# Kernel optimization log

Hardware: AMD Instinct MI355X
Metric: run time of the kernel (lower is better)

## Reference

```python
import jax, jax.numpy as jnp
import numpy as np

B, L, H, NH = 2, 256, 512, 8
DH = H // NH
MAXLEN = 256           # module's max_seq_len; pe index offset
PE_ROWS = 2 * MAXLEN + 1


def _lin(x, W, b):
    # torch nn.Linear convention: y = x @ W.T + b
    return x @ W.T + b


def setup_inputs() -> dict:
    rng = jax.random.key(0)
    ks = jax.random.split(rng, 24)
    s = 0.02
    inp = {
        "key": jax.random.normal(ks[0], (B, L, H), jnp.float32),
        "query": jax.random.normal(ks[1], (B, L, H), jnp.float32),
        "value": jax.random.normal(ks[2], (B, L, H), jnp.float32),
        # learned params
        "pe": jax.random.normal(ks[3], (PE_ROWS, H), jnp.float32) * s,
        "Wf": jax.random.normal(ks[4], (H, 4 * H), jnp.float32) * s,
        "bf": jnp.zeros((H,), jnp.float32),
        "Wk": jax.random.normal(ks[5], (H, H), jnp.float32) * s,
        "bk": jnp.zeros((H,), jnp.float32),
        "Wq": jax.random.normal(ks[6], (H, H), jnp.float32) * s,
        "bq": jnp.zeros((H,), jnp.float32),
        "Wv": jax.random.normal(ks[7], (H, H), jnp.float32) * s,
        "bv": jnp.zeros((H,), jnp.float32),
        "Wr": jax.random.normal(ks[8], (H, H), jnp.float32) * s,
        "br": jnp.zeros((H,), jnp.float32),
        "Wo": jax.random.normal(ks[9], (H, H), jnp.float32) * s,  # ff_final
        "bo": jnp.zeros((H,), jnp.float32),
        "u": jax.random.normal(ks[10], (NH, DH), jnp.float32) * s,
        "v": jax.random.normal(ks[11], (NH, DH), jnp.float32) * s,
        # int inputs
        "seq_len": jax.random.randint(ks[12], (B,), 100, 200).astype(jnp.int64),
        "lex_num": jax.random.randint(ks[13], (B,), 0, 50).astype(jnp.int64),
    }
    pos_s = jax.random.randint(ks[14], (B, L), 0, 250)
    pos_e = pos_s + jax.random.randint(ks[15], (B, L), 0, 5)
    inp["pos_s"] = pos_s.astype(jnp.int64)
    inp["pos_e"] = pos_e.astype(jnp.int64)
    return inp


def reference(key, query, value, pe, Wf, bf, Wk, bk, Wq, bq, Wv, bv, Wr, br,
              Wo, bo, u, v, seq_len, lex_num, pos_s, pos_e):
    b, l, _ = key.shape
    # four relative position matrices [B, L, L]
    pos_ss = pos_s[:, :, None] - pos_s[:, None, :]
    pos_se = pos_s[:, :, None] - pos_e[:, None, :]
    pos_es = pos_e[:, :, None] - pos_s[:, None, :]
    pos_ee = pos_e[:, :, None] - pos_e[:, None, :]
    # gather pe embeddings, each [B, L, L, H]
    pe_ss = pe[pos_ss + MAXLEN]
    pe_se = pe[pos_se + MAXLEN]
    pe_es = pe[pos_es + MAXLEN]
    pe_ee = pe[pos_ee + MAXLEN]
    pe_4 = jnp.concatenate([pe_ss, pe_se, pe_es, pe_ee], axis=-1)  # [B,L,L,4H]
    rel = jax.nn.relu(_lin(pe_4, Wf, bf))                          # 'ff' fusion -> [B,L,L,H]

    q = _lin(query, Wq, bq).reshape(b, l, NH, DH).transpose(0, 2, 1, 3)  # [B,nh,L,dh]
    k = _lin(key, Wk, bk).reshape(b, l, NH, DH).transpose(0, 2, 1, 3)
    val = _lin(value, Wv, bv).reshape(b, l, NH, DH).transpose(0, 2, 1, 3)
    rel = _lin(rel, Wr, br).reshape(b, l, l, NH, DH)               # [B,L,L,nh,dh]

    A = jnp.einsum('bhid,bhjd->bhij', q, k)
    B_ = jnp.einsum('bhid,bijhd->bhij', q, rel)
    C = jnp.einsum('hd,bhjd->bhj', u, k)[:, :, None, :]
    D = jnp.einsum('hd,bijhd->bhij', v, rel)

    score = (A + B_ + C + D) / np.float32(np.sqrt(DH))
    total_len = seq_len + lex_num                                   # [B]
    mask = (jnp.arange(l)[None, :] < total_len[:, None])[:, None, None, :]
    score = jnp.where(mask, score, jnp.float32(-1e15))
    attn = jax.nn.softmax(score, axis=-1)
    out = jnp.einsum('bhij,bhjd->bhid', attn, val)                  # [B,nh,L,dh]
    out = out.transpose(0, 2, 1, 3).reshape(b, l, H)
    return _lin(out, Wo, bo)
```

## Files before the change

### kernel.cpp

```cpp
#include <hip/hip_runtime.h>
#include <hip/hip_bf16.h>

typedef unsigned short USHORT;
typedef long long LL;
typedef short s8v __attribute__((ext_vector_type(8)));
typedef float f32x4 __attribute__((ext_vector_type(4)));


__device__ __forceinline__ float bf2f(USHORT u) {
  union { unsigned int i; float f; } v; v.i = ((unsigned int)u) << 16; return v.f;
}
__device__ __forceinline__ USHORT f2bf(float f) {
  unsigned int x = __float_as_uint(f);
  return (USHORT)((x + 0x7fffu + ((x >> 16) & 1u)) >> 16);
}

struct PrepArgs {
  const void* fsrc[18]; USHORT* fdst[18]; int fn[18];
  const void* wr_src; USHORT* wrT;
  const void* isrc[4]; int* idst[4];
};

__global__ __launch_bounds__(256) void prep_k(PrepArgs a, const void* qraw, int* flags) {
  __shared__ int s_w;
  const int t = threadIdx.x;
  if (t == 0) s_w = 0;
  __syncthreads();
  const USHORT* qb = (const USHORT*)qraw;
  int wild = 0;
  for (int c = t; c < 512; c += 256) {
    float x = bf2f(qb[c]);
    if (!(fabsf(x) <= 1024.0f)) wild = 1;
  }
  if (wild) atomicAdd(&s_w, 1);
  __syncthreads();
  const int f = (s_w == 0) ? 1 : 0;

  const int y = blockIdx.y;
  if (y < 18) {
    const int n = a.fn[y];
    const USHORT* sb = (const USHORT*)a.fsrc[y];
    const float* sf = (const float*)a.fsrc[y];
    USHORT* d = a.fdst[y];
    for (int idx = blockIdx.x * 256 + t; idx < n; idx += gridDim.x * 256)
      d[idx] = f ? sb[idx] : f2bf(sf[idx]);
  } else if (y == 18) {
    const USHORT* sb = (const USHORT*)a.wr_src;
    const float* sf = (const float*)a.wr_src;
    for (int idx = blockIdx.x * 256 + t; idx < 262144; idx += gridDim.x * 256) {
      const int e = idx >> 9, dd = idx & 511;
      const int s = dd * 512 + e;
      a.wrT[idx] = f ? sb[s] : f2bf(sf[s]);
    }
  } else if (blockIdx.x == 0) {
    if (t == 0) flags[0] = f;
    const int fi = (((const int*)a.isrc[0])[1] == 0) ? 1 : 0;
    if (t < 2) {
      a.idst[0][t] = fi ? (int)((const LL*)a.isrc[0])[t] : ((const int*)a.isrc[0])[t];
      a.idst[1][t] = fi ? (int)((const LL*)a.isrc[1])[t] : ((const int*)a.isrc[1])[t];
    }
    for (int c = t; c < 512; c += 256) {
      a.idst[2][c] = fi ? (int)((const LL*)a.isrc[2])[c] : ((const int*)a.isrc[2])[c];
      a.idst[3][c] = fi ? (int)((const LL*)a.isrc[3])[c] : ((const int*)a.isrc[3])[c];
    }
  }
}

struct GDesc {
  const USHORT* A; const USHORT* W; const USHORT* bias;
  void* out;
  int M, N, K, lda, ldw, koff, ldo, mode, trans, pad;
};
struct GArgs { GDesc d[32]; };

__global__ __launch_bounds__(256) void gemm2_k(GArgs ga, const int* __restrict__ flags) {
  const GDesc de = ga.d[blockIdx.z];
  const int row0 = blockIdx.y * 64, col0 = blockIdx.x * 64;
  if (row0 >= de.M || col0 >= de.N) return;
  const int wave = threadIdx.x >> 6, lane = threadIdx.x & 63;
  const int mrow = row0 + wave * 16 + (lane & 15);
  const int kq = (lane >> 4) * 8;
  const bool mok = (mrow < de.M);
  const USHORT* ar = de.A + (long)(mok ? mrow : row0) * de.lda + kq;
  const int nc = col0 + (lane & 15);
  const USHORT* w0p = de.W + (long)(nc +  0) * de.ldw + de.koff + kq;
  const USHORT* w1p = de.W + (long)(nc + 16) * de.ldw + de.koff + kq;
  const USHORT* w2p = de.W + (long)(nc + 32) * de.ldw + de.koff + kq;
  const USHORT* w3p = de.W + (long)(nc + 48) * de.ldw + de.koff + kq;

  f32x4 acc[4] = {};
#pragma unroll 4
  for (int k0 = 0; k0 < de.K; k0 += 32) {
    s8v a = *(const s8v*)(ar + k0);
    s8v wv0 = *(const s8v*)(w0p + k0);
    s8v wv1 = *(const s8v*)(w1p + k0);
    s8v wv2 = *(const s8v*)(w2p + k0);
    s8v wv3 = *(const s8v*)(w3p + k0);
    acc[0] = __builtin_amdgcn_mfma_f32_16x16x32_bf16(a, wv0, acc[0], 0, 0, 0);
    acc[1] = __builtin_amdgcn_mfma_f32_16x16x32_bf16(a, wv1, acc[1], 0, 0, 0);
    acc[2] = __builtin_amdgcn_mfma_f32_16x16x32_bf16(a, wv2, acc[2], 0, 0, 0);
    acc[3] = __builtin_amdgcn_mfma_f32_16x16x32_bf16(a, wv3, acc[3], 0, 0, 0);
  }

  const int obf = (de.mode == 2) ? flags[0] : (de.mode == 1);
  const int mbase = row0 + wave * 16 + (lane >> 4) * 4;
#pragma unroll
  for (int nt = 0; nt < 4; nt++) {
    const int n = col0 + nt * 16 + (lane & 15);
    const float bias = de.bias ? bf2f(de.bias[n]) : 0.f;
#pragma unroll
    for (int r = 0; r < 4; r++) {
      const int m = mbase + r;
      if (m >= de.M) continue;
      const float vo = acc[nt][r] + bias;
      const long off = de.trans ? ((long)n * de.ldo + m) : ((long)m * de.ldo + n);
      if (obf) ((USHORT*)de.out)[off] = f2bf(vo);
      else     ((float*)de.out)[off] = vo;
    }
  }
}

__global__ __launch_bounds__(256) void mid_k(
    const USHORT* __restrict__ Ptab, const USHORT* __restrict__ q_n,
    const USHORT* __restrict__ k_n, const USHORT* __restrict__ WrT,
    const USHORT* __restrict__ u_bf, const USHORT* __restrict__ v_bf,
    const USHORT* __restrict__ br_bf,
    USHORT* __restrict__ T,
    float* __restrict__ cbv, float* __restrict__ uk, USHORT* __restrict__ vwr)
{
  const int bid = blockIdx.x, t = threadIdx.x, gsz = gridDim.x;
  const long TS = 513l * 512;
  for (int r = bid; r < 12825; r += gsz) {
    const int S0 = r / 25, rem = r % 25, di = rem / 5, dj = rem % 5;
    const USHORT* p1 = Ptab + (long)S0 * 512;
    const USHORT* p2 = Ptab + TS + (long)max(S0 - dj, 0) * 512;
    const USHORT* p3 = Ptab + 2 * TS + (long)min(S0 + di, 512) * 512;
    const USHORT* p4 = Ptab + 3 * TS + (long)min(max(S0 + di - dj, 0), 512) * 512;
    USHORT* to = T + (long)r * 512;
    const int e = t * 2;
    ushort2 x1 = *(const ushort2*)(p1 + e);
    ushort2 x2 = *(const ushort2*)(p2 + e);
    ushort2 x3 = *(const ushort2*)(p3 + e);
    ushort2 x4 = *(const ushort2*)(p4 + e);
    ushort2 o;
    o.x = f2bf(fmaxf(bf2f(x1.x) + bf2f(x2.x) + bf2f(x3.x) + bf2f(x4.x), 0.f));
    o.y = f2bf(fmaxf(bf2f(x1.y) + bf2f(x2.y) + bf2f(x3.y) + bf2f(x4.y), 0.f));
    *(ushort2*)(to + e) = o;
  }
  for (int idx = bid * 256 + t; idx < 262144; idx += gsz * 256) {
    const int hd = idx & 511;
    float s = (bf2f(q_n[idx]) + bf2f(v_bf[hd])) * bf2f(br_bf[hd]);
    float s2 = bf2f(k_n[idx]) * bf2f(u_bf[hd]);
#pragma unroll
    for (int off = 32; off > 0; off >>= 1) { s += __shfl_xor(s, off); s2 += __shfl_xor(s2, off); }
    if ((t & 63) == 0) { cbv[idx >> 6] = s; uk[idx >> 6] = s2; }
  }
  for (int o = bid * 256 + t; o < 4096; o += gsz * 256) {
    const int h = o >> 9, e = o & 511;
    float s = 0.f;
    const USHORT* wrow = WrT + (long)e * 512 + h * 64;
    const USHORT* vrow = v_bf + h * 64;
#pragma unroll
    for (int d = 0; d < 64; d += 4) {
      ushort4 wv = *(const ushort4*)(wrow + d);
      ushort4 vv = *(const ushort4*)(vrow + d);
      s += bf2f(vv.x) * bf2f(wv.x) + bf2f(vv.y) * bf2f(wv.y) +
           bf2f(vv.z) * bf2f(wv.z) + bf2f(vv.w) * bf2f(wv.w);
    }
    vwr[o] = f2bf(s);
  }
}

__global__ __launch_bounds__(1024) void score6_k(
    const USHORT* __restrict__ T,
    const float* __restrict__ cbv, const float* __restrict__ uk,
    const USHORT* __restrict__ wbuf, const float* __restrict__ S_AC,
    const USHORT* __restrict__ v_t,
    const int* __restrict__ seq_len, const int* __restrict__ lex_num,
    const int* __restrict__ pos_s, const int* __restrict__ pos_e,
    USHORT* __restrict__ out_pre)
{
  __shared__ float att[8 * 256];
  __shared__ float red[4][4];
  const int i = blockIdx.x, b = blockIdx.y, t = threadIdx.x;
  const int wave = t >> 6, lane = t & 63;
  int tl = seq_len[b] + lex_num[b];
  tl = min(max(tl, 1), 256);

  const int j0 = wave * 16;
  if (j0 < tl) {
    const int n = lane & 15, q = lane >> 4;
    const int psi = pos_s[b * 256 + i], pei = pos_e[b * 256 + i];
    const int j = j0 + n;
    const int psj = pos_s[b * 256 + j], pej = pos_e[b * 256 + j];
    const int S0 = min(max(psi - psj + 256, 0), 512);
    const int di = min(max(pei - psi, 0), 4);
    const int dj = min(max(pej - psj, 0), 4);
    const USHORT* tp = T + ((long)(S0 * 25 + di * 5 + dj)) * 512 + q * 8;
    const USHORT* wr = wbuf + ((long)((b * 8 + (n & 7)) * 256 + i)) * 512 + q * 8;
    f32x4 acc = {0.f, 0.f, 0.f, 0.f};
#pragma unroll
    for (int kk = 0; kk < 16; kk++) {
      s8v av = *(const s8v*)(tp + kk * 32);
      s8v wv = *(const s8v*)(wr + kk * 32);
      acc = __builtin_amdgcn_mfma_f32_16x16x32_bf16(av, wv, acc, 0, 0, 0);
    }
    if (n < 8) {
      const long base = (long)(b * 8 + n) * 256 + i;
      const float cb = cbv[(long)(b * 256 + i) * 8 + n];
      const float4 sac = *(const float4*)(S_AC + base * 256 + j0 + q * 4);
      const float* sacp = (const float*)&sac;
#pragma unroll
      for (int r = 0; r < 4; r++) {
        const int jr = j0 + q * 4 + r;
        att[n * 256 + jr] = (acc[r] + sacp[r] + cb + uk[(long)(b * 256 + jr) * 8 + n]) * 0.125f;
      }
    }
  }
  __syncthreads();

  const int hg = t >> 8, tj = t & 255, wig = wave & 3;
#pragma unroll
  for (int hh = 0; hh < 2; hh++) {
    const int h = hg + 4 * hh;
    const float val = (tj < tl) ? att[h * 256 + tj] : -3.0e38f;
    float m = val;
#pragma unroll
    for (int off = 32; off > 0; off >>= 1) m = fmaxf(m, __shfl_xor(m, off));
    if (lane == 0) red[hg][wig] = m;
    __syncthreads();
    m = fmaxf(fmaxf(red[hg][0], red[hg][1]), fmaxf(red[hg][2], red[hg][3]));
    const float pv = (tj < tl) ? __expf(val - m) : 0.f;
    float s = pv;
#pragma unroll
    for (int off = 32; off > 0; off >>= 1) s += __shfl_xor(s, off);
    __syncthreads();
    if (lane == 0) red[hg][wig] = s;
    __syncthreads();
    s = red[hg][0] + red[hg][1] + red[hg][2] + red[hg][3];
    if (!(s > 1e-30f)) s = 1.f;
    att[h * 256 + tj] = pv / s;
    __syncthreads();
  }

  if (t < 512) {
    const int h = t >> 6, d = t & 63;
    const USHORT* vrow = v_t + (long)(h * 64 + d) * 512 + b * 256;
    const float* arow = &att[h * 256];
    float acc = 0.f;
    const int tl4 = (tl + 3) & ~3;
    for (int jj = 0; jj < tl4; jj += 4) {
      ushort4 vv = *(const ushort4*)(vrow + jj);
      acc += arow[jj + 0] * bf2f(vv.x) + arow[jj + 1] * bf2f(vv.y) +
             arow[jj + 2] * bf2f(vv.z) + arow[jj + 3] * bf2f(vv.w);
    }
    out_pre[(long)(b * 256 + i) * 512 + h * 64 + d] = f2bf(acc);
  }
}

extern "C" void kernel_launch(void* const* d_in, const int* in_sizes, int n_in,
                              void* d_out, int out_size, void* d_ws, size_t ws_size,
                              hipStream_t stream) {
  (void)in_sizes; (void)n_in; (void)out_size; (void)ws_size;

  char* w = (char*)d_ws;
  auto take = [&](size_t n) { char* r = w; w += (n + 255) & ~(size_t)255; return r; };

  int* flags   = (int*)take(16);
  int* c_seq   = (int*)take(16);
  int* c_lex   = (int*)take(16);
  int* c_pos_s = (int*)take(2048);
  int* c_pos_e = (int*)take(2048);
  const int ns[18] = {262144,262144,262144,262656,1048576,512,262144,512,262144,512,
                      262144,512,262144,512,262144,512,512,512};
  USHORT* canon[18];
  for (int i = 0; i < 18; i++) canon[i] = (USHORT*)take((size_t)ns[i] * 2);
  USHORT* WrT     = (USHORT*)take((size_t)262144 * 2);
  USHORT* q_n     = (USHORT*)take((size_t)262144 * 2);
  USHORT* k_n     = (USHORT*)take((size_t)262144 * 2);
  USHORT* v_t     = (USHORT*)take((size_t)262144 * 2);
  USHORT* wbuf    = (USHORT*)take((size_t)2097152 * 2);
  USHORT* Ptab    = (USHORT*)take((size_t)1050624 * 2);
  USHORT* T       = (USHORT*)take((size_t)12825 * 512 * 2);
  USHORT* vwr     = (USHORT*)take((size_t)4096 * 2);
  USHORT* out_pre = (USHORT*)take((size_t)262144 * 2);
  float* S   = (float*)take((size_t)1048576 * 4);
  float* cbv = (float*)take((size_t)4096 * 4);
  float* uk  = (float*)take((size_t)4096 * 4);

  PrepArgs pa;
  for (int i = 0; i < 18; i++) { pa.fsrc[i] = d_in[i]; pa.fdst[i] = canon[i]; pa.fn[i] = ns[i]; }
  pa.wr_src = d_in[12]; pa.wrT = WrT;
  for (int i = 0; i < 4; i++) pa.isrc[i] = d_in[18 + i];
  pa.idst[0] = c_seq; pa.idst[1] = c_lex; pa.idst[2] = c_pos_s; pa.idst[3] = c_pos_e;
  prep_k<<<dim3(64, 20), 256, 0, stream>>>(pa, d_in[1], flags);

  GArgs gA = {};
  for (int z = 0; z < 4; z++)
    gA.d[z] = {canon[3], canon[4], (z == 0) ? canon[5] : nullptr, Ptab + (long)z * 513 * 512,
               513, 512, 512, 512, 2048, z * 512, 512, 1, 0, 0};
  gA.d[4] = {canon[1], canon[8],  canon[9],  q_n, 512, 512, 512, 512, 512, 0, 512, 1, 0, 0};
  gA.d[5] = {canon[0], canon[6],  canon[7],  k_n, 512, 512, 512, 512, 512, 0, 512, 1, 0, 0};
  gA.d[6] = {canon[2], canon[10], canon[11], v_t, 512, 512, 512, 512, 512, 0, 512, 1, 1, 0};
  gemm2_k<<<dim3(8, 9, 7), 256, 0, stream>>>(gA, flags);

  mid_k<<<512, 256, 0, stream>>>(Ptab, q_n, k_n, WrT, canon[16], canon[17], canon[13],
                                 T, cbv, uk, vwr);

  GArgs gB = {};
  for (int z = 0; z < 16; z++) {
    const int b = z >> 3, h = z & 7;
    gB.d[z] = {q_n + b * 131072 + h * 64, WrT, vwr + h * 512, wbuf + (long)z * 131072,
               256, 512, 64, 512, 512, h * 64, 512, 1, 0, 0};
  }
  for (int z = 0; z < 16; z++) {
    const int b = z >> 3, h = z & 7;
    gB.d[16 + z] = {q_n + b * 131072 + h * 64, k_n + b * 131072 + h * 64, nullptr,
                    S + (long)z * 65536, 256, 256, 64, 512, 512, 0, 256, 0, 0, 0};
  }
  gemm2_k<<<dim3(8, 4, 32), 256, 0, stream>>>(gB, flags);

  score6_k<<<dim3(256, 2), 1024, 0, stream>>>(
      T, cbv, uk, wbuf, S, v_t, c_seq, c_lex, c_pos_s, c_pos_e, out_pre);

  GArgs gC = {};
  gC.d[0] = {out_pre, canon[14], canon[15], d_out, 512, 512, 512, 512, 512, 0, 512, 2, 0, 0};
  gemm2_k<<<dim3(8, 8, 1), 256, 0, stream>>>(gC, flags);
}
```

Baseline: 216.8 us.

## Merge mid-stage elementwise work into the batched GEMM launch and move vWr into prep

Removes the separate mid_k launch. Its T-table build and the cbv/uk reductions now run in extra blocks of a combined g2mid_k kernel, alongside the per-head GEMM tiles, using a hand-mapped block index. The v·Wr product (vwr) is computed in a new prep_k block row that reads raw Wr directly, and the unused canonical Wr copy is skipped. This cuts one kernel launch and its serialization, and lets the independent elementwise work overlap with the GEMMs. The cost is a strided, uncoalesced read of Wr in prep and fixed block partitioning inside the combined kernel.

```diff
diff --git a/kernel.cpp b/kernel.cpp
--- a/kernel.cpp
+++ b/kernel.cpp
@@ -17,7 +17,7 @@
 
 struct PrepArgs {
   const void* fsrc[18]; USHORT* fdst[18]; int fn[18];
-  const void* wr_src; USHORT* wrT;
+  const void* wr_src; USHORT* wrT; USHORT* vwr;
   const void* isrc[4]; int* idst[4];
 };
 
@@ -38,6 +38,7 @@
 
   const int y = blockIdx.y;
   if (y < 18) {
+    if (y == 12) return;
     const int n = a.fn[y];
     const USHORT* sb = (const USHORT*)a.fsrc[y];
     const float* sf = (const float*)a.fsrc[y];
@@ -52,6 +53,29 @@
       const int s = dd * 512 + e;
       a.wrT[idx] = f ? sb[s] : f2bf(sf[s]);
     }
+  } else if (y == 19) {
+    const int o = blockIdx.x * 256 + t;
+    if (o < 4096) {
+      const int h = o >> 9, e = o & 511;
+      const USHORT* wb = (const USHORT*)a.wr_src;
+      const float* wf = (const float*)a.wr_src;
+      const USHORT* vb = (const USHORT*)a.fsrc[17];
+      const float* vf = (const float*)a.fsrc[17];
+      float s = 0.f;
+#pragma unroll 4
+      for (int d = 0; d < 64; d += 4) {
+        float acc4 = 0.f;
+#pragma unroll
+        for (int dd = 0; dd < 4; dd++) {
+          const int hd = h * 64 + d + dd;
+          const float vv = bf2f(f ? vb[hd] : f2bf(vf[hd]));
+          const float wv = bf2f(f ? wb[(long)hd * 512 + e] : f2bf(wf[(long)hd * 512 + e]));
+          acc4 += vv * wv;
+        }
+        s += acc4;
+      }
+      a.vwr[o] = f2bf(s);
+    }
   } else if (blockIdx.x == 0) {
     if (t == 0) flags[0] = f;
     const int fi = (((const int*)a.isrc[0])[1] == 0) ? 1 : 0;
@@ -73,11 +97,10 @@
 };
 struct GArgs { GDesc d[32]; };
 
-__global__ __launch_bounds__(256) void gemm2_k(GArgs ga, const int* __restrict__ flags) {
-  const GDesc de = ga.d[blockIdx.z];
-  const int row0 = blockIdx.y * 64, col0 = blockIdx.x * 64;
+__device__ __forceinline__ void gemm_tile(const GDesc& de, int row0, int col0, int t,
+                                          const int* __restrict__ flags) {
   if (row0 >= de.M || col0 >= de.N) return;
-  const int wave = threadIdx.x >> 6, lane = threadIdx.x & 63;
+  const int wave = t >> 6, lane = t & 63;
   const int mrow = row0 + wave * 16 + (lane & 15);
   const int kq = (lane >> 4) * 8;
   const bool mok = (mrow < de.M);
@@ -120,54 +143,52 @@
   }
 }
 
-__global__ __launch_bounds__(256) void mid_k(
-    const USHORT* __restrict__ Ptab, const USHORT* __restrict__ q_n,
-    const USHORT* __restrict__ k_n, const USHORT* __restrict__ WrT,
+__global__ __launch_bounds__(256) void gemm2_k(GArgs ga, const int* __restrict__ flags) {
+  gemm_tile(ga.d[blockIdx.z], blockIdx.y * 64, blockIdx.x * 64, threadIdx.x, flags);
+}
+
+__global__ __launch_bounds__(256) void g2mid_k(
+    GArgs ga, const USHORT* __restrict__ Ptab,
+    const USHORT* __restrict__ q_n, const USHORT* __restrict__ k_n,
     const USHORT* __restrict__ u_bf, const USHORT* __restrict__ v_bf,
     const USHORT* __restrict__ br_bf,
-    USHORT* __restrict__ T,
-    float* __restrict__ cbv, float* __restrict__ uk, USHORT* __restrict__ vwr)
+    USHORT* __restrict__ T, float* __restrict__ cbv, float* __restrict__ uk,
+    const int* __restrict__ flags)
 {
-  const int bid = blockIdx.x, t = threadIdx.x, gsz = gridDim.x;
-  const long TS = 513l * 512;
-  for (int r = bid; r < 12825; r += gsz) {
-    const int S0 = r / 25, rem = r % 25, di = rem / 5, dj = rem % 5;
-    const USHORT* p1 = Ptab + (long)S0 * 512;
-    const USHORT* p2 = Ptab + TS + (long)max(S0 - dj, 0) * 512;
-    const USHORT* p3 = Ptab + 2 * TS + (long)min(S0 + di, 512) * 512;
-    const USHORT* p4 = Ptab + 3 * TS + (long)min(max(S0 + di - dj, 0), 512) * 512;
-    USHORT* to = T + (long)r * 512;
-    const int e = t * 2;
-    ushort2 x1 = *(const ushort2*)(p1 + e);
-    ushort2 x2 = *(const ushort2*)(p2 + e);
-    ushort2 x3 = *(const ushort2*)(p3 + e);
-    ushort2 x4 = *(const ushort2*)(p4 + e);
-    ushort2 o;
-    o.x = f2bf(fmaxf(bf2f(x1.x) + bf2f(x2.x) + bf2f(x3.x) + bf2f(x4.x), 0.f));
-    o.y = f2bf(fmaxf(bf2f(x1.y) + bf2f(x2.y) + bf2f(x3.y) + bf2f(x4.y), 0.f));
-    *(ushort2*)(to + e) = o;
-  }
-  for (int idx = bid * 256 + t; idx < 262144; idx += gsz * 256) {
-    const int hd = idx & 511;
-    float s = (bf2f(q_n[idx]) + bf2f(v_bf[hd])) * bf2f(br_bf[hd]);
-    float s2 = bf2f(k_n[idx]) * bf2f(u_bf[hd]);
-#pragma unroll
-    for (int off = 32; off > 0; off >>= 1) { s += __shfl_xor(s, off); s2 += __shfl_xor(s2, off); }
-    if ((t & 63) == 0) { cbv[idx >> 6] = s; uk[idx >> 6] = s2; }
-  }
-  for (int o = bid * 256 + t; o < 4096; o += gsz * 256) {
-    const int h = o >> 9, e = o & 511;
-    float s = 0.f;
-    const USHORT* wrow = WrT + (long)e * 512 + h * 64;
-    const USHORT* vrow = v_bf + h * 64;
-#pragma unroll
-    for (int d = 0; d < 64; d += 4) {
-      ushort4 wv = *(const ushort4*)(wrow + d);
-      ushort4 vv = *(const ushort4*)(vrow + d);
-      s += bf2f(vv.x) * bf2f(wv.x) + bf2f(vv.y) * bf2f(wv.y) +
-           bf2f(vv.z) * bf2f(wv.z) + bf2f(vv.w) * bf2f(wv.w);
-    }
-    vwr[o] = f2bf(s);
+  const int bid = blockIdx.x, t = threadIdx.x;
+  if (bid < 768) {
+    int z, uy, ux;
+    if (bid < 512) { z = bid >> 5; const int tile = bid & 31; ux = tile >> 2; uy = tile & 3; }
+    else { const int b2 = bid - 512; z = 16 + (b2 >> 4); const int tile = b2 & 15; ux = tile >> 2; uy = tile & 3; }
+    gemm_tile(ga.d[z], uy * 64, ux * 64, t, flags);
+  } else if (bid < 896) {
+    const long TS = 513l * 512;
+    for (int r = bid - 768; r < 12825; r += 128) {
+      const int S0 = r / 25, rem = r % 25, di = rem / 5, dj = rem % 5;
+      const USHORT* p1 = Ptab + (long)S0 * 512;
+      const USHORT* p2 = Ptab + TS + (long)max(S0 - dj, 0) * 512;
+      const USHORT* p3 = Ptab + 2 * TS + (long)min(S0 + di, 512) * 512;
+      const USHORT* p4 = Ptab + 3 * TS + (long)min(max(S0 + di - dj, 0), 512) * 512;
+      USHORT* to = T + (long)r * 512;
+      const int e = t * 2;
+      ushort2 x1 = *(const ushort2*)(p1 + e);
+      ushort2 x2 = *(const ushort2*)(p2 + e);
+      ushort2 x3 = *(const ushort2*)(p3 + e);
+      ushort2 x4 = *(const ushort2*)(p4 + e);
+      ushort2 o;
+      o.x = f2bf(fmaxf(bf2f(x1.x) + bf2f(x2.x) + bf2f(x3.x) + bf2f(x4.x), 0.f));
+      o.y = f2bf(fmaxf(bf2f(x1.y) + bf2f(x2.y) + bf2f(x3.y) + bf2f(x4.y), 0.f));
+      *(ushort2*)(to + e) = o;
+    }
+  } else {
+    for (int idx = (bid - 896) * 256 + t; idx < 262144; idx += 64 * 256) {
+      const int hd = idx & 511;
+      float s = (bf2f(q_n[idx]) + bf2f(v_bf[hd])) * bf2f(br_bf[hd]);
+      float s2 = bf2f(k_n[idx]) * bf2f(u_bf[hd]);
+#pragma unroll
+      for (int off = 32; off > 0; off >>= 1) { s += __shfl_xor(s, off); s2 += __shfl_xor(s2, off); }
+      if ((t & 63) == 0) { cbv[idx >> 6] = s; uk[idx >> 6] = s2; }
+    }
   }
 }
 
@@ -274,7 +295,7 @@
   const int ns[18] = {262144,262144,262144,262656,1048576,512,262144,512,262144,512,
                       262144,512,262144,512,262144,512,512,512};
   USHORT* canon[18];
-  for (int i = 0; i < 18; i++) canon[i] = (USHORT*)take((size_t)ns[i] * 2);
+  for (int i = 0; i < 18; i++) canon[i] = (USHORT*)take(i == 12 ? 1024 : (size_t)ns[i] * 2);
   USHORT* WrT     = (USHORT*)take((size_t)262144 * 2);
   USHORT* q_n     = (USHORT*)take((size_t)262144 * 2);
   USHORT* k_n     = (USHORT*)take((size_t)262144 * 2);
@@ -290,10 +311,10 @@
 
   PrepArgs pa;
   for (int i = 0; i < 18; i++) { pa.fsrc[i] = d_in[i]; pa.fdst[i] = canon[i]; pa.fn[i] = ns[i]; }
-  pa.wr_src = d_in[12]; pa.wrT = WrT;
+  pa.wr_src = d_in[12]; pa.wrT = WrT; pa.vwr = vwr;
   for (int i = 0; i < 4; i++) pa.isrc[i] = d_in[18 + i];
   pa.idst[0] = c_seq; pa.idst[1] = c_lex; pa.idst[2] = c_pos_s; pa.idst[3] = c_pos_e;
-  prep_k<<<dim3(64, 20), 256, 0, stream>>>(pa, d_in[1], flags);
+  prep_k<<<dim3(64, 21), 256, 0, stream>>>(pa, d_in[1], flags);
 
   GArgs gA = {};
   for (int z = 0; z < 4; z++)
@@ -304,9 +325,6 @@
   gA.d[6] = {canon[2], canon[10], canon[11], v_t, 512, 512, 512, 512, 512, 0, 512, 1, 1, 0};
   gemm2_k<<<dim3(8, 9, 7), 256, 0, stream>>>(gA, flags);
 
-  mid_k<<<512, 256, 0, stream>>>(Ptab, q_n, k_n, WrT, canon[16], canon[17], canon[13],
-                                 T, cbv, uk, vwr);
-
   GArgs gB = {};
   for (int z = 0; z < 16; z++) {
     const int b = z >> 3, h = z & 7;
@@ -318,7 +336,8 @@
     gB.d[16 + z] = {q_n + b * 131072 + h * 64, k_n + b * 131072 + h * 64, nullptr,
                     S + (long)z * 65536, 256, 256, 64, 512, 512, 0, 256, 0, 0, 0};
   }
-  gemm2_k<<<dim3(8, 4, 32), 256, 0, stream>>>(gB, flags);
+  g2mid_k<<<960, 256, 0, stream>>>(gB, Ptab, q_n, k_n, canon[16], canon[17], canon[13],
+                                   T, cbv, uk, flags);
 
   score6_k<<<dim3(256, 2), 1024, 0, stream>>>(
       T, cbv, uk, wbuf, S, v_t, c_seq, c_lex, c_pos_s, c_pos_e, out_pre);
```

Result: no change. 220.8 us (+1.9%).
